# Optimization experiments

Measured on AMD Instinct MI355X. Metric: run time of the kernel, lower is better.

Reference implementation:

```python
import jax, jax.numpy as jnp
import numpy as np
from jax import lax

U, K, POOL, STRIDE, FC = 300, 19, 7, 7, 100   # num_units, filter size, maxpool, fc_size
B, L, D = 256, 1000, 4                        # batch, seq len, DNA dim
P = (L - (K - 1) - (POOL - 1) - 1) // STRIDE + 1  # post_pool_size = 140
EPS = 1e-5  # BatchNorm eps (eval mode with running stats; Dropout is identity in eval)


def setup_inputs() -> dict:
    key = jax.random.key(0)
    ks = jax.random.split(key, 24)
    rn = lambda k, shp, s=0.1: jax.random.normal(k, shp, jnp.float32) * s
    return {
        "input_seq": jax.random.normal(ks[0], (B, L, D), jnp.float32),
        # per-unit conv (groups=U on tiled input == plain Conv1d(4, U, K))
        "w_conv": rn(ks[1], (U, D, K)), "b_conv": rn(ks[2], (U,)),
        "g1": 1.0 + rn(ks[3], (U,)), "be1": rn(ks[4], (U,)),
        "m1": rn(ks[5], (U,)), "v1": 1.0 + jax.random.uniform(ks[6], (U,), jnp.float32),
        # per-unit FC1 (grouped 1x1 conv: P -> FC per unit)
        "w_fc1": rn(ks[7], (U, FC, P)), "b_fc1": rn(ks[8], (U, FC)),
        "g2": 1.0 + rn(ks[9], (U, FC)), "be2": rn(ks[10], (U, FC)),
        "m2": rn(ks[11], (U, FC)), "v2": 1.0 + jax.random.uniform(ks[12], (U, FC), jnp.float32),
        # per-unit FC2 (grouped 1x1 conv: FC -> 1 per unit)
        "w_fc2": rn(ks[13], (U, FC)), "b_fc2": rn(ks[14], (U,)),
        "g3": 1.0 + rn(ks[15], (U,)), "be3": rn(ks[16], (U,)),
        "m3": rn(ks[17], (U,)), "v3": 1.0 + jax.random.uniform(ks[18], (U,), jnp.float32),
        # final Linear(U, 1)
        "w_out": rn(ks[19], (U, 1)), "b_out": rn(ks[20], (1,)),
    }


def reference(input_seq, w_conv, b_conv, g1, be1, m1, v1, w_fc1, b_fc1,
              g2, be2, m2, v2, w_fc2, b_fc2, g3, be3, m3, v3, w_out, b_out):
    x = jnp.transpose(input_seq, (0, 2, 1))  # B,D,L
    # grouped conv on input tiled U times: every group sees the same D=4 channels,
    # so it is exactly a plain Conv1d(D, U, K).
    conv = lax.conv_general_dilated(
        x, w_conv, (1,), 'VALID', dimension_numbers=('NCH', 'OIH', 'NCH')
    ) + b_conv[None, :, None]                 # B,U,L' (L'=L-K+1)
    a = (conv - m1[None, :, None]) * (g1 / jnp.sqrt(v1 + EPS))[None, :, None] + be1[None, :, None]
    a = jnp.exp(a)
    pooled = lax.reduce_window(a, -jnp.inf, lax.max,
                               (1, 1, POOL), (1, 1, STRIDE), 'VALID')  # B,U,P
    # Flatten->Unsqueeze->grouped 1x1 conv == per-unit matmul over P
    h = jnp.einsum('bup,ufp->buf', pooled, w_fc1) + b_fc1               # B,U,FC
    h = jax.nn.relu((h - m2) * (g2 / jnp.sqrt(v2 + EPS)) + be2)
    z = jnp.einsum('buf,uf->bu', h, w_fc2) + b_fc2                      # B,U
    z = jax.nn.relu((z - m3) * (g3 / jnp.sqrt(v3 + EPS)) + be3)
    return jax.nn.sigmoid(z @ w_out + b_out)                            # B,1
```

## Files before the change

kernel.cpp:

```cpp
#include <hip/hip_runtime.h>
#include <hip/hip_bf16.h>
#include <math.h>

#define U_   300
#define K_   19
#define FC_  100
#define B_   256
#define L_   1000
#define P_   140
#define EPS_ 1e-5f
#define UP_  128
#define KP_  144

typedef unsigned short ushort_t;
typedef __attribute__((ext_vector_type(8)))  short short8v;
typedef __attribute__((ext_vector_type(16))) float f32x16;

__device__ __forceinline__ ushort_t f2bf(float f) {
    union { float f; unsigned u; } a; a.f = f;
    unsigned r = a.u + 0x7fffu + ((a.u >> 16) & 1u);
    return (ushort_t)(r >> 16);
}

__global__ __launch_bounds__(256, 4)
void pack_all_k(const float* __restrict__ w_conv, const float* __restrict__ b_conv,
                const float* __restrict__ g1, const float* __restrict__ be1,
                const float* __restrict__ m1, const float* __restrict__ v1,
                const float* __restrict__ w_fc1, const float* __restrict__ b_fc1,
                const float* __restrict__ g2, const float* __restrict__ be2,
                const float* __restrict__ m2, const float* __restrict__ v2,
                const float* __restrict__ w_fc2,
                ushort_t* __restrict__ w_bf, float* __restrict__ o1g,
                ushort_t* __restrict__ w1p, float* __restrict__ o2p,
                float* __restrict__ w2p)
{
    const int t = blockIdx.x * 256 + threadIdx.x;
    if (t < U_ * UP_ * KP_) {
        const int u = t / (UP_ * KP_);
        const int r = t - u * (UP_ * KP_);
        const int f = r / KP_;
        const int k = r - f * KP_;
        float val = 0.f;
        if (f < FC_ && k < P_) {
            const int fg = u * FC_ + f;
            const float s2 = g2[fg] / sqrtf(v2[fg] + EPS_);
            val = w_fc1[(size_t)fg * P_ + k] * s2;
        }
        w1p[t] = f2bf(val);
    }
    if (t < U_ * UP_) {
        const int u = t / UP_, f = t - u * UP_;
        float o2 = 0.f, w2 = 0.f;
        if (f < FC_) {
            const int fg = u * FC_ + f;
            const float s2 = g2[fg] / sqrtf(v2[fg] + EPS_);
            o2 = (b_fc1[fg] - m2[fg]) * s2 + be2[fg];
            w2 = w_fc2[fg];
        }
        o2p[t] = o2;
        w2p[t] = w2;
    }
    if (t < 320 * 80) {
        const int u = t / 80, j = t - u * 80;
        float val = 0.f;
        if (u < U_ && j < 76) {
            const int tp = j >> 2;
            const int d  = j & 3;
            const float s1 = g1[u] / sqrtf(v1[u] + EPS_);
            val = w_conv[u * 76 + 19 * d + tp] * s1;
        }
        w_bf[t] = f2bf(val);
    }
    if (t < 320) {
        float o = 0.f;
        if (t < U_) {
            const float s1 = g1[t] / sqrtf(v1[t] + EPS_);
            o = (b_conv[t] - m1[t]) * s1 + be1[t];
        }
        o1g[t] = o;
    }
}

__global__ __launch_bounds__(256, 2)
void conv_mfma_k(const float4* __restrict__ x4,
                 const ushort_t* __restrict__ w_bf,
                 const float* __restrict__ o1g,
                 ushort_t* __restrict__ pooled)
{
    __shared__ ushort_t xls[880];
    const int tid = threadIdx.x;
    const int b   = blockIdx.y;
    const int bx  = blockIdx.x;
    const int w0  = bx * 28;
    const int l0  = w0 * 7;

    if (tid < 220) {
        const int gi = l0 + tid;
        float4 v = make_float4(0.f, 0.f, 0.f, 0.f);
        if (gi < L_) v = x4[(size_t)b * L_ + gi];
        ushort4 pk;
        pk.x = f2bf(v.x); pk.y = f2bf(v.y); pk.z = f2bf(v.z); pk.w = f2bf(v.w);
        *(ushort4*)&xls[4 * tid] = pk;
    }
    __syncthreads();

    const int lane = tid & 63;
    const int wv   = tid >> 6;
    const int half = lane >> 5;
    const int r32  = lane & 31;
    const bool hasB = (wv < 3);
    const int tA = 2 * wv;
    const int tB = hasB ? (2 * wv + 1) : 0;

    const int sreg = (r32 & 3) + 4 * (r32 >> 3);
    const int sh   = (r32 >> 2) & 1;
    const int off  = sreg < 7  ? sreg + 7 * sh
                   : sreg < 14 ? sreg + 7 + 7 * sh
                               : 28 + (sreg - 14) + 2 * sh;

    const char* xbA = (const char*)xls + 8 * (28 * tA + off) + 16 * half;
    const char* xbB = (const char*)xls + 8 * (28 * tB + off) + 16 * half;
    const char* wbase = (const char*)w_bf + 16 * half + 160 * r32;

    short8v aA[5], aB[5];
#pragma unroll
    for (int kc = 0; kc < 5; ++kc) {
        aA[kc] = *(const short8v*)(xbA + 32 * kc);
        aB[kc] = *(const short8v*)(xbB + 32 * kc);
    }

    const int pA = w0 + 8 * wv;
    const int pB = pA + 4;

    short8v bfr[5];
#pragma unroll
    for (int kc = 0; kc < 5; ++kc)
        bfr[kc] = *(const short8v*)(wbase + 32 * kc);
    float o1u = o1g[r32];

    for (int nt = 0; nt < 10; ++nt) {
        const int ntn = (nt < 9) ? nt + 1 : nt;
        short8v bnx[5];
        const char* wn = wbase + ntn * 5120;
#pragma unroll
        for (int kc = 0; kc < 5; ++kc)
            bnx[kc] = *(const short8v*)(wn + 32 * kc);
        const float o1n = o1g[ntn * 32 + r32];

        f32x16 accA = {};
#pragma unroll
        for (int kc = 0; kc < 5; ++kc)
            accA = __builtin_amdgcn_mfma_f32_32x32x16_bf16(aA[kc], bfr[kc], accA, 0, 0, 0);
        f32x16 accB = {};
        if (hasB) {
#pragma unroll
            for (int kc = 0; kc < 5; ++kc)
                accB = __builtin_amdgcn_mfma_f32_32x32x16_bf16(aB[kc], bfr[kc], accB, 0, 0, 0);
        }

        float mA0 = accA[0], mA1 = accA[7];
#pragma unroll
        for (int j = 1; j < 7; ++j)  mA0 = fmaxf(mA0, accA[j]);
#pragma unroll
        for (int j = 8; j < 14; ++j) mA1 = fmaxf(mA1, accA[j]);
        const unsigned pkA = (unsigned)f2bf(__expf(mA0 + o1u)) |
                             ((unsigned)f2bf(__expf(mA1 + o1u)) << 16);
        const unsigned oA = __shfl_xor(pkA, 32);

        const int u = nt * 32 + r32;
        if (u < U_ && half == 0) {
            ushort4 st;
            st.x = (ushort_t)(pkA & 0xffff);
            st.y = (ushort_t)(oA  & 0xffff);
            st.z = (ushort_t)(pkA >> 16);
            st.w = (ushort_t)(oA  >> 16);
            *(ushort4*)&pooled[((size_t)u * B_ + b) * P_ + pA] = st;
        }

        if (hasB) {
            float mB0 = accB[0], mB1 = accB[7];
#pragma unroll
            for (int j = 1; j < 7; ++j)  mB0 = fmaxf(mB0, accB[j]);
#pragma unroll
            for (int j = 8; j < 14; ++j) mB1 = fmaxf(mB1, accB[j]);
            const unsigned pkB = (unsigned)f2bf(__expf(mB0 + o1u)) |
                                 ((unsigned)f2bf(__expf(mB1 + o1u)) << 16);
            const unsigned oB = __shfl_xor(pkB, 32);
            if (u < U_ && half == 1) {
                ushort4 st;
                st.x = (ushort_t)(oB  & 0xffff);
                st.y = (ushort_t)(pkB & 0xffff);
                st.z = (ushort_t)(oB  >> 16);
                st.w = (ushort_t)(pkB >> 16);
                *(ushort4*)&pooled[((size_t)u * B_ + b) * P_ + pB] = st;
            }
        }

#pragma unroll
        for (int kc = 0; kc < 5; ++kc) bfr[kc] = bnx[kc];
        o1u = o1n;
    }
}

__global__ __launch_bounds__(256, 3)
void fc_mfma_k(const ushort_t* __restrict__ pooled,
               const ushort_t* __restrict__ w1p,
               const float* __restrict__ o2p,
               const float* __restrict__ w2p,
               const float* __restrict__ b_fc2,
               const float* __restrict__ g3,
               const float* __restrict__ be3,
               const float* __restrict__ m3,
               const float* __restrict__ v3,
               float* __restrict__ zT)
{
    __shared__ float zred[128][33];
    const int tid  = threadIdx.x;
    const int u    = blockIdx.y;
    const int bt   = blockIdx.x;
    const int lane = tid & 63;
    const int wv   = tid >> 6;
    const int half = lane >> 5;
    const int r32  = lane & 31;

    const int brow = bt * 128 + wv * 32 + r32;
    const ushort_t* __restrict__ abase =
        pooled + ((size_t)u * B_ + brow) * P_ + half * 8;
    const ushort_t* __restrict__ bbase =
        w1p + ((size_t)u * UP_ + r32) * KP_ + half * 8;

    short8v ac  = *(const short8v*)(abase);
    short8v b0c = *(const short8v*)(bbase);
    short8v b1c = *(const short8v*)(bbase + 32 * KP_);
    short8v b2c = *(const short8v*)(bbase + 64 * KP_);
    short8v b3c = *(const short8v*)(bbase + 96 * KP_);

    f32x16 acc0 = {}, acc1 = {}, acc2 = {}, acc3 = {};
#pragma unroll
    for (int kc = 0; kc < 9; ++kc) {
        const int kn = (kc < 8) ? kc + 1 : kc;
        const short8v an  = *(const short8v*)(abase + kn * 16);
        const short8v b0n = *(const short8v*)(bbase            + kn * 16);
        const short8v b1n = *(const short8v*)(bbase + 32 * KP_ + kn * 16);
        const short8v b2n = *(const short8v*)(bbase + 64 * KP_ + kn * 16);
        const short8v b3n = *(const short8v*)(bbase + 96 * KP_ + kn * 16);
        acc0 = __builtin_amdgcn_mfma_f32_32x32x16_bf16(ac, b0c, acc0, 0, 0, 0);
        acc1 = __builtin_amdgcn_mfma_f32_32x32x16_bf16(ac, b1c, acc1, 0, 0, 0);
        acc2 = __builtin_amdgcn_mfma_f32_32x32x16_bf16(ac, b2c, acc2, 0, 0, 0);
        acc3 = __builtin_amdgcn_mfma_f32_32x32x16_bf16(ac, b3c, acc3, 0, 0, 0);
        ac = an; b0c = b0n; b1c = b1n; b2c = b2n; b3c = b3n;
    }

    const int fb = u * UP_ + r32;
    const float o20 = o2p[fb],      w20 = w2p[fb];
    const float o21 = o2p[fb + 32], w21 = w2p[fb + 32];
    const float o22 = o2p[fb + 64], w22 = w2p[fb + 64];
    const float o23 = o2p[fb + 96], w23 = w2p[fb + 96];
#pragma unroll
    for (int rg = 0; rg < 16; ++rg) {
        const int row = (rg & 3) + 8 * (rg >> 2) + 4 * half;
        float s = fmaxf(acc0[rg] + o20, 0.f) * w20;
        s = fmaf(fmaxf(acc1[rg] + o21, 0.f), w21, s);
        s = fmaf(fmaxf(acc2[rg] + o22, 0.f), w22, s);
        s = fmaf(fmaxf(acc3[rg] + o23, 0.f), w23, s);
        zred[wv * 32 + row][r32] = s;
    }
    __syncthreads();

    if (tid < 128) {
        float s = 0.f;
#pragma unroll
        for (int j = 0; j < 32; ++j) s += zred[tid][j];
        const float s3 = g3[u] / sqrtf(v3[u] + EPS_);
        const float o3 = (b_fc2[u] - m3[u]) * s3 + be3[u];
        zT[(size_t)(bt * 128 + tid) * 304 + u] = fmaxf(fmaf(s, s3, o3), 0.f);
    }
}

__global__ __launch_bounds__(64, 8)
void out_k(const float* __restrict__ zT,
           const float* __restrict__ w_out,
           const float* __restrict__ b_out,
           float* __restrict__ out)
{
    const int lane = threadIdx.x;
    const int b    = blockIdx.x;
    const float4* zr = (const float4*)(zT + (size_t)b * 304);
    const float4* w4 = (const float4*)w_out;

    float s = 0.f;
    for (int i = lane; i < 75; i += 64) {
        const float4 z = zr[i], w = w4[i];
        s += z.x * w.x + z.y * w.y + z.z * w.z + z.w * w.w;
    }
#pragma unroll
    for (int o = 32; o > 0; o >>= 1) s += __shfl_xor(s, o);
    if (lane == 0)
        out[b] = 1.0f / (1.0f + __expf(-(s + b_out[0])));
}

extern "C" void kernel_launch(void* const* d_in, const int* in_sizes, int n_in,
                              void* d_out, int out_size, void* d_ws, size_t ws_size,
                              hipStream_t stream)
{
    const float* input_seq = (const float*)d_in[0];
    const float* w_conv    = (const float*)d_in[1];
    const float* b_conv    = (const float*)d_in[2];
    const float* g1        = (const float*)d_in[3];
    const float* be1       = (const float*)d_in[4];
    const float* m1        = (const float*)d_in[5];
    const float* v1        = (const float*)d_in[6];
    const float* w_fc1     = (const float*)d_in[7];
    const float* b_fc1     = (const float*)d_in[8];
    const float* g2        = (const float*)d_in[9];
    const float* be2       = (const float*)d_in[10];
    const float* m2        = (const float*)d_in[11];
    const float* v2        = (const float*)d_in[12];
    const float* w_fc2     = (const float*)d_in[13];
    const float* b_fc2     = (const float*)d_in[14];
    const float* g3        = (const float*)d_in[15];
    const float* be3       = (const float*)d_in[16];
    const float* m3        = (const float*)d_in[17];
    const float* v3        = (const float*)d_in[18];
    const float* w_out     = (const float*)d_in[19];
    const float* b_out     = (const float*)d_in[20];

    char* p = (char*)d_ws;
    ushort_t* pooled = (ushort_t*)p;                 p += (size_t)B_ * U_ * P_ * 2;
    ushort_t* w1p    = (ushort_t*)p;                 p += (size_t)U_ * UP_ * KP_ * 2;
    float*    o2p    = (float*)p;                    p += (size_t)U_ * UP_ * 4;
    float*    w2p    = (float*)p;                    p += (size_t)U_ * UP_ * 4;
    ushort_t* w_bf   = (ushort_t*)p;                 p += 320 * 80 * 2;
    float*    o1g    = (float*)p;                    p += 320 * 4;
    float*    zT     = (float*)p;                    p += (size_t)B_ * 304 * 4;

    pack_all_k<<<dim3((U_ * UP_ * KP_ + 255) / 256), 256, 0, stream>>>(
        w_conv, b_conv, g1, be1, m1, v1,
        w_fc1, b_fc1, g2, be2, m2, v2, w_fc2,
        w_bf, o1g, w1p, o2p, w2p);

    conv_mfma_k<<<dim3(5, B_), 256, 0, stream>>>(
        (const float4*)input_seq, w_bf, o1g, pooled);

    fc_mfma_k<<<dim3(2, U_), 256, 0, stream>>>(
        pooled, w1p, o2p, w2p, b_fc2, g3, be3, m3, v3, zT);

    out_k<<<dim3(B_), 64, 0, stream>>>(zT, w_out, b_out, (float*)d_out);
}
```

Before: 63.26 us.

## Fuse FC1 weight packing into FC kernel and widen conv blocks to 7 waves

The large pre-pass that packed the FC1 weights into bf16 with the BN2 scale folded in is removed. Each FC block now converts its unit's weights to bf16 in LDS and applies the BN2 scale and offset in the epilogue instead. This removes a full write and re-read of the packed weight buffer plus most of the pack launch, but every FC block (two per unit) now redoes the conversion. The conv kernel also moves from 4 waves each handling two pooled tiles to 7 waves handling one tile each, for more parallelism and fewer registers per thread.

```diff
diff --git a/kernel.cpp b/kernel.cpp
--- a/kernel.cpp
+++ b/kernel.cpp
@@ -9,8 +9,7 @@
 #define L_   1000
 #define P_   140
 #define EPS_ 1e-5f
-#define UP_  128
-#define KP_  144
+#define WLD_ 144
 
 typedef unsigned short ushort_t;
 typedef __attribute__((ext_vector_type(8)))  short short8v;
@@ -23,43 +22,12 @@
 }
 
 __global__ __launch_bounds__(256, 4)
-void pack_all_k(const float* __restrict__ w_conv, const float* __restrict__ b_conv,
-                const float* __restrict__ g1, const float* __restrict__ be1,
-                const float* __restrict__ m1, const float* __restrict__ v1,
-                const float* __restrict__ w_fc1, const float* __restrict__ b_fc1,
-                const float* __restrict__ g2, const float* __restrict__ be2,
-                const float* __restrict__ m2, const float* __restrict__ v2,
-                const float* __restrict__ w_fc2,
-                ushort_t* __restrict__ w_bf, float* __restrict__ o1g,
-                ushort_t* __restrict__ w1p, float* __restrict__ o2p,
-                float* __restrict__ w2p)
+void pack_conv_k(const float* __restrict__ w_conv, const float* __restrict__ b_conv,
+                 const float* __restrict__ g1, const float* __restrict__ be1,
+                 const float* __restrict__ m1, const float* __restrict__ v1,
+                 ushort_t* __restrict__ w_bf, float* __restrict__ o1g)
 {
     const int t = blockIdx.x * 256 + threadIdx.x;
-    if (t < U_ * UP_ * KP_) {
-        const int u = t / (UP_ * KP_);
-        const int r = t - u * (UP_ * KP_);
-        const int f = r / KP_;
-        const int k = r - f * KP_;
-        float val = 0.f;
-        if (f < FC_ && k < P_) {
-            const int fg = u * FC_ + f;
-            const float s2 = g2[fg] / sqrtf(v2[fg] + EPS_);
-            val = w_fc1[(size_t)fg * P_ + k] * s2;
-        }
-        w1p[t] = f2bf(val);
-    }
-    if (t < U_ * UP_) {
-        const int u = t / UP_, f = t - u * UP_;
-        float o2 = 0.f, w2 = 0.f;
-        if (f < FC_) {
-            const int fg = u * FC_ + f;
-            const float s2 = g2[fg] / sqrtf(v2[fg] + EPS_);
-            o2 = (b_fc1[fg] - m2[fg]) * s2 + be2[fg];
-            w2 = w_fc2[fg];
-        }
-        o2p[t] = o2;
-        w2p[t] = w2;
-    }
     if (t < 320 * 80) {
         const int u = t / 80, j = t - u * 80;
         float val = 0.f;
@@ -81,7 +49,7 @@
     }
 }
 
-__global__ __launch_bounds__(256, 2)
+__global__ __launch_bounds__(448, 3)
 void conv_mfma_k(const float4* __restrict__ x4,
                  const ushort_t* __restrict__ w_bf,
                  const float* __restrict__ o1g,
@@ -108,9 +76,6 @@
     const int wv   = tid >> 6;
     const int half = lane >> 5;
     const int r32  = lane & 31;
-    const bool hasB = (wv < 3);
-    const int tA = 2 * wv;
-    const int tB = hasB ? (2 * wv + 1) : 0;
 
     const int sreg = (r32 & 3) + 4 * (r32 >> 3);
     const int sh   = (r32 >> 2) & 1;
@@ -118,19 +83,15 @@
                    : sreg < 14 ? sreg + 7 + 7 * sh
                                : 28 + (sreg - 14) + 2 * sh;
 
-    const char* xbA = (const char*)xls + 8 * (28 * tA + off) + 16 * half;
-    const char* xbB = (const char*)xls + 8 * (28 * tB + off) + 16 * half;
+    const char* xb    = (const char*)xls + 8 * (28 * wv + off) + 16 * half;
     const char* wbase = (const char*)w_bf + 16 * half + 160 * r32;
 
-    short8v aA[5], aB[5];
-#pragma unroll
-    for (int kc = 0; kc < 5; ++kc) {
-        aA[kc] = *(const short8v*)(xbA + 32 * kc);
-        aB[kc] = *(const short8v*)(xbB + 32 * kc);
-    }
-
-    const int pA = w0 + 8 * wv;
-    const int pB = pA + 4;
+    short8v aA[5];
+#pragma unroll
+    for (int kc = 0; kc < 5; ++kc)
+        aA[kc] = *(const short8v*)(xb + 32 * kc);
+
+    const int pA = w0 + 4 * wv;
 
     short8v bfr[5];
 #pragma unroll
@@ -147,55 +108,30 @@
             bnx[kc] = *(const short8v*)(wn + 32 * kc);
         const float o1n = o1g[ntn * 32 + r32];
 
-        f32x16 accA = {};
+        f32x16 acc = {};
 #pragma unroll
         for (int kc = 0; kc < 5; ++kc)
-            accA = __builtin_amdgcn_mfma_f32_32x32x16_bf16(aA[kc], bfr[kc], accA, 0, 0, 0);
-        f32x16 accB = {};
-        if (hasB) {
-#pragma unroll
-            for (int kc = 0; kc < 5; ++kc)
-                accB = __builtin_amdgcn_mfma_f32_32x32x16_bf16(aB[kc], bfr[kc], accB, 0, 0, 0);
-        }
-
-        float mA0 = accA[0], mA1 = accA[7];
-#pragma unroll
-        for (int j = 1; j < 7; ++j)  mA0 = fmaxf(mA0, accA[j]);
-#pragma unroll
-        for (int j = 8; j < 14; ++j) mA1 = fmaxf(mA1, accA[j]);
-        const unsigned pkA = (unsigned)f2bf(__expf(mA0 + o1u)) |
-                             ((unsigned)f2bf(__expf(mA1 + o1u)) << 16);
-        const unsigned oA = __shfl_xor(pkA, 32);
+            acc = __builtin_amdgcn_mfma_f32_32x32x16_bf16(aA[kc], bfr[kc], acc, 0, 0, 0);
+
+        float m0 = acc[0], m1 = acc[7];
+#pragma unroll
+        for (int j = 1; j < 7; ++j)  m0 = fmaxf(m0, acc[j]);
+#pragma unroll
+        for (int j = 8; j < 14; ++j) m1 = fmaxf(m1, acc[j]);
+        const unsigned pk = (unsigned)f2bf(__expf(m0 + o1u)) |
+                            ((unsigned)f2bf(__expf(m1 + o1u)) << 16);
+        const unsigned ot = __shfl_xor(pk, 32);
 
         const int u = nt * 32 + r32;
         if (u < U_ && half == 0) {
             ushort4 st;
-            st.x = (ushort_t)(pkA & 0xffff);
-            st.y = (ushort_t)(oA  & 0xffff);
-            st.z = (ushort_t)(pkA >> 16);
-            st.w = (ushort_t)(oA  >> 16);
+            st.x = (ushort_t)(pk & 0xffff);
+            st.y = (ushort_t)(ot & 0xffff);
+            st.z = (ushort_t)(pk >> 16);
+            st.w = (ushort_t)(ot >> 16);
             *(ushort4*)&pooled[((size_t)u * B_ + b) * P_ + pA] = st;
         }
 
-        if (hasB) {
-            float mB0 = accB[0], mB1 = accB[7];
-#pragma unroll
-            for (int j = 1; j < 7; ++j)  mB0 = fmaxf(mB0, accB[j]);
-#pragma unroll
-            for (int j = 8; j < 14; ++j) mB1 = fmaxf(mB1, accB[j]);
-            const unsigned pkB = (unsigned)f2bf(__expf(mB0 + o1u)) |
-                                 ((unsigned)f2bf(__expf(mB1 + o1u)) << 16);
-            const unsigned oB = __shfl_xor(pkB, 32);
-            if (u < U_ && half == 1) {
-                ushort4 st;
-                st.x = (ushort_t)(oB  & 0xffff);
-                st.y = (ushort_t)(pkB & 0xffff);
-                st.z = (ushort_t)(oB  >> 16);
-                st.w = (ushort_t)(pkB >> 16);
-                *(ushort4*)&pooled[((size_t)u * B_ + b) * P_ + pB] = st;
-            }
-        }
-
 #pragma unroll
         for (int kc = 0; kc < 5; ++kc) bfr[kc] = bnx[kc];
         o1u = o1n;
@@ -204,9 +140,13 @@
 
 __global__ __launch_bounds__(256, 3)
 void fc_mfma_k(const ushort_t* __restrict__ pooled,
-               const ushort_t* __restrict__ w1p,
-               const float* __restrict__ o2p,
-               const float* __restrict__ w2p,
+               const float* __restrict__ w_fc1,
+               const float* __restrict__ b_fc1,
+               const float* __restrict__ g2,
+               const float* __restrict__ be2,
+               const float* __restrict__ m2,
+               const float* __restrict__ v2,
+               const float* __restrict__ w_fc2,
                const float* __restrict__ b_fc2,
                const float* __restrict__ g3,
                const float* __restrict__ be3,
@@ -214,10 +154,26 @@
                const float* __restrict__ v3,
                float* __restrict__ zT)
 {
+    __shared__ ushort_t wlds[FC_ * WLD_];
     __shared__ float zred[128][33];
     const int tid  = threadIdx.x;
     const int u    = blockIdx.y;
     const int bt   = blockIdx.x;
+
+    const float* __restrict__ wsrc = w_fc1 + (size_t)u * FC_ * P_;
+    for (int idx = tid; idx < FC_ * 35; idx += 256) {
+        const int f = idx / 35, j = idx - f * 35;
+        const float4 v = *(const float4*)(wsrc + f * P_ + 4 * j);
+        ushort4 pk;
+        pk.x = f2bf(v.x); pk.y = f2bf(v.y); pk.z = f2bf(v.z); pk.w = f2bf(v.w);
+        *(ushort4*)&wlds[f * WLD_ + 4 * j] = pk;
+    }
+    for (int idx = tid; idx < FC_ * 4; idx += 256) {
+        const int f = idx >> 2, k = 140 + (idx & 3);
+        wlds[f * WLD_ + k] = 0;
+    }
+    __syncthreads();
+
     const int lane = tid & 63;
     const int wv   = tid >> 6;
     const int half = lane >> 5;
@@ -226,43 +182,51 @@
     const int brow = bt * 128 + wv * 32 + r32;
     const ushort_t* __restrict__ abase =
         pooled + ((size_t)u * B_ + brow) * P_ + half * 8;
-    const ushort_t* __restrict__ bbase =
-        w1p + ((size_t)u * UP_ + r32) * KP_ + half * 8;
-
-    short8v ac  = *(const short8v*)(abase);
-    short8v b0c = *(const short8v*)(bbase);
-    short8v b1c = *(const short8v*)(bbase + 32 * KP_);
-    short8v b2c = *(const short8v*)(bbase + 64 * KP_);
-    short8v b3c = *(const short8v*)(bbase + 96 * KP_);
-
+
+    const ushort_t* __restrict__ bl0 = &wlds[r32 * WLD_ + half * 8];
+    const ushort_t* __restrict__ bl1 = &wlds[(32 + r32) * WLD_ + half * 8];
+    const ushort_t* __restrict__ bl2 = &wlds[(64 + r32) * WLD_ + half * 8];
+    const int f3c = (96 + r32 < FC_) ? (96 + r32) : (FC_ - 1);
+    const ushort_t* __restrict__ bl3 = &wlds[f3c * WLD_ + half * 8];
+
+    short8v ac = *(const short8v*)(abase);
     f32x16 acc0 = {}, acc1 = {}, acc2 = {}, acc3 = {};
 #pragma unroll
     for (int kc = 0; kc < 9; ++kc) {
         const int kn = (kc < 8) ? kc + 1 : kc;
-        const short8v an  = *(const short8v*)(abase + kn * 16);
-        const short8v b0n = *(const short8v*)(bbase            + kn * 16);
-        const short8v b1n = *(const short8v*)(bbase + 32 * KP_ + kn * 16);
-        const short8v b2n = *(const short8v*)(bbase + 64 * KP_ + kn * 16);
-        const short8v b3n = *(const short8v*)(bbase + 96 * KP_ + kn * 16);
-        acc0 = __builtin_amdgcn_mfma_f32_32x32x16_bf16(ac, b0c, acc0, 0, 0, 0);
-        acc1 = __builtin_amdgcn_mfma_f32_32x32x16_bf16(ac, b1c, acc1, 0, 0, 0);
-        acc2 = __builtin_amdgcn_mfma_f32_32x32x16_bf16(ac, b2c, acc2, 0, 0, 0);
-        acc3 = __builtin_amdgcn_mfma_f32_32x32x16_bf16(ac, b3c, acc3, 0, 0, 0);
-        ac = an; b0c = b0n; b1c = b1n; b2c = b2n; b3c = b3n;
-    }
-
-    const int fb = u * UP_ + r32;
-    const float o20 = o2p[fb],      w20 = w2p[fb];
-    const float o21 = o2p[fb + 32], w21 = w2p[fb + 32];
-    const float o22 = o2p[fb + 64], w22 = w2p[fb + 64];
-    const float o23 = o2p[fb + 96], w23 = w2p[fb + 96];
+        const short8v an = *(const short8v*)(abase + kn * 16);
+        const short8v b0 = *(const short8v*)(bl0 + kc * 16);
+        const short8v b1 = *(const short8v*)(bl1 + kc * 16);
+        const short8v b2 = *(const short8v*)(bl2 + kc * 16);
+        const short8v b3 = *(const short8v*)(bl3 + kc * 16);
+        acc0 = __builtin_amdgcn_mfma_f32_32x32x16_bf16(ac, b0, acc0, 0, 0, 0);
+        acc1 = __builtin_amdgcn_mfma_f32_32x32x16_bf16(ac, b1, acc1, 0, 0, 0);
+        acc2 = __builtin_amdgcn_mfma_f32_32x32x16_bf16(ac, b2, acc2, 0, 0, 0);
+        acc3 = __builtin_amdgcn_mfma_f32_32x32x16_bf16(ac, b3, acc3, 0, 0, 0);
+        ac = an;
+    }
+
+    float s2[4], o2[4], w2[4];
+#pragma unroll
+    for (int n = 0; n < 4; ++n) {
+        const int f = n * 32 + r32;
+        if (f < FC_) {
+            const int fg = u * FC_ + f;
+            const float ss = g2[fg] / sqrtf(v2[fg] + EPS_);
+            s2[n] = ss;
+            o2[n] = (b_fc1[fg] - m2[fg]) * ss + be2[fg];
+            w2[n] = w_fc2[fg];
+        } else {
+            s2[n] = 0.f; o2[n] = 0.f; w2[n] = 0.f;
+        }
+    }
 #pragma unroll
     for (int rg = 0; rg < 16; ++rg) {
         const int row = (rg & 3) + 8 * (rg >> 2) + 4 * half;
-        float s = fmaxf(acc0[rg] + o20, 0.f) * w20;
-        s = fmaf(fmaxf(acc1[rg] + o21, 0.f), w21, s);
-        s = fmaf(fmaxf(acc2[rg] + o22, 0.f), w22, s);
-        s = fmaf(fmaxf(acc3[rg] + o23, 0.f), w23, s);
+        float s = fmaxf(fmaf(acc0[rg], s2[0], o2[0]), 0.f) * w2[0];
+        s = fmaf(fmaxf(fmaf(acc1[rg], s2[1], o2[1]), 0.f), w2[1], s);
+        s = fmaf(fmaxf(fmaf(acc2[rg], s2[2], o2[2]), 0.f), w2[2], s);
+        s = fmaf(fmaxf(fmaf(acc3[rg], s2[3], o2[3]), 0.f), w2[3], s);
         zred[wv * 32 + row][r32] = s;
     }
     __syncthreads();
@@ -326,24 +290,20 @@
     const float* b_out     = (const float*)d_in[20];
 
     char* p = (char*)d_ws;
-    ushort_t* pooled = (ushort_t*)p;                 p += (size_t)B_ * U_ * P_ * 2;
-    ushort_t* w1p    = (ushort_t*)p;                 p += (size_t)U_ * UP_ * KP_ * 2;
-    float*    o2p    = (float*)p;                    p += (size_t)U_ * UP_ * 4;
-    float*    w2p    = (float*)p;                    p += (size_t)U_ * UP_ * 4;
-    ushort_t* w_bf   = (ushort_t*)p;                 p += 320 * 80 * 2;
-    float*    o1g    = (float*)p;                    p += 320 * 4;
-    float*    zT     = (float*)p;                    p += (size_t)B_ * 304 * 4;
-
-    pack_all_k<<<dim3((U_ * UP_ * KP_ + 255) / 256), 256, 0, stream>>>(
-        w_conv, b_conv, g1, be1, m1, v1,
-        w_fc1, b_fc1, g2, be2, m2, v2, w_fc2,
-        w_bf, o1g, w1p, o2p, w2p);
-
-    conv_mfma_k<<<dim3(5, B_), 256, 0, stream>>>(
+    ushort_t* pooled = (ushort_t*)p;   p += (size_t)B_ * U_ * P_ * 2;
+    ushort_t* w_bf   = (ushort_t*)p;   p += 320 * 80 * 2;
+    float*    o1g    = (float*)p;      p += 320 * 4;
+    float*    zT     = (float*)p;      p += (size_t)B_ * 304 * 4;
+
+    pack_conv_k<<<dim3(100), 256, 0, stream>>>(
+        w_conv, b_conv, g1, be1, m1, v1, w_bf, o1g);
+
+    conv_mfma_k<<<dim3(5, B_), 448, 0, stream>>>(
         (const float4*)input_seq, w_bf, o1g, pooled);
 
     fc_mfma_k<<<dim3(2, U_), 256, 0, stream>>>(
-        pooled, w1p, o2p, w2p, b_fc2, g3, be3, m3, v3, zT);
+        pooled, w_fc1, b_fc1, g2, be2, m2, v2, w_fc2, b_fc2,
+        g3, be3, m3, v3, zT);
 
     out_k<<<dim3(B_), 64, 0, stream>>>(zT, w_out, b_out, (float*)d_out);
 }
```

New measurement: 62.18 us. No clear change (-1.7%).
